# Optimization experiments

Measured on AMD Instinct MI355X. Metric: run time of the kernel, lower is better.

## Reference

```python
import jax, jax.numpy as jnp
import numpy as np

S, B, D, V = 1024, 8, 512, 8000


def _ln(x, g, b, eps=1e-5):
    m = x.mean(-1, keepdims=True)
    v = x.var(-1, keepdims=True)
    return (x - m) / jnp.sqrt(v + eps) * g + b


def setup_inputs() -> dict:
    key = jax.random.key(0)
    ks = jax.random.split(key, 8)
    representation = jax.random.normal(ks[0], (S, B, D), jnp.float32)
    # CTC-style logits: tokens come in runs of ~4 frames so argmax has segments
    tok = jax.random.randint(ks[1], (S // 4, B), 0, V)
    tok = jnp.repeat(tok, 4, axis=0)  # [S,B]
    logit = jax.random.normal(ks[2], (S, B, V), jnp.float32) + 6.0 * jax.nn.one_hot(tok, V, dtype=jnp.float32)
    padding = jnp.zeros((B, S), bool)  # all frames valid
    # linear_adapter: Linear(D,2D) -> ReLU -> Linear(2D,D) -> LayerNorm
    w1 = jax.random.normal(ks[3], (2 * D, D), jnp.float32) * (D ** -0.5)
    b1 = jnp.zeros((2 * D,), jnp.float32)
    w2 = jax.random.normal(ks[4], (D, 2 * D), jnp.float32) * ((2 * D) ** -0.5)
    b2 = jnp.zeros((D,), jnp.float32)
    ln1_g = jnp.ones((D,), jnp.float32)
    ln1_b = jnp.zeros((D,), jnp.float32)
    # embed_adapter weight [dict_size, dim], init std = dim**-0.5
    emb_w = jax.random.normal(ks[5], (V, D), jnp.float32) * (D ** -0.5)
    eln_g = jnp.ones((D,), jnp.float32)
    eln_b = jnp.zeros((D,), jnp.float32)
    return dict(representation=representation, logit=logit, padding=padding,
                w1=w1, b1=b1, w2=w2, b2=b2, ln1_g=ln1_g, ln1_b=ln1_b,
                emb_w=emb_w, eln_g=eln_g, eln_b=eln_b)


def reference(representation, logit, padding, w1, b1, w2, b2, ln1_g, ln1_b, emb_w, eln_g, eln_b):
    # distribution = softmax(logit / T), T = 1.0
    dist = jax.nn.softmax(logit, axis=-1)  # [S,B,V]
    # linear adapter: Linear -> ReLU -> Linear -> LN
    h = jax.nn.relu(jnp.einsum('sbd,ed->sbe', representation, w1) + b1)
    linear_out = _ln(jnp.einsum('sbe,de->sbd', h, w2) + b2, ln1_g, ln1_b)
    # context adapter: dist @ embed_adapter.weight, then embed LN
    soft_out = _ln(jnp.einsum('sbv,vd->sbd', dist, emb_w), eln_g, eln_b)
    out = linear_out + soft_out  # league
    # --- CTC 'avg' compress (shrink), vectorized; output padded to S frames ---
    pred = jnp.argmax(dist, axis=-1).T  # [B,S]
    valid = ~padding  # [B,S]
    prev = jnp.concatenate([jnp.full((pred.shape[0], 1), -1, pred.dtype), pred[:, :-1]], axis=1)
    change = (pred != prev) & valid  # segment starts
    seg = jnp.cumsum(change, axis=1) - 1  # segment id per frame
    seg = jnp.where(valid, seg, S)  # invalid frames -> out-of-range id
    # weights_matrix[b, t, s] = 1/len(segment s) if frame t in segment s
    onehot = (seg[:, :, None] == jnp.arange(S)[None, None, :]).astype(out.dtype)  # [B,S,S]
    counts = onehot.sum(1)  # [B,S] frames per segment
    w = onehot * jnp.where(counts > 0, 1.0 / counts, 0.0)[:, None, :]
    # representation.permute(1,2,0).bmm(weights).permute(2,0,1)
    compressed = jnp.einsum('sbd,bst->tbd', out, w)  # [S_new(padded to S), B, D]
    new_lengths = change.sum(1)
    new_padding = jnp.arange(S)[None, :] >= new_lengths[:, None]
    return compressed, new_padding
```

## Files before the change

kernel.cpp:

```cpp
#include <hip/hip_runtime.h>
#include <hip/hip_bf16.h>

typedef __attribute__((ext_vector_type(8))) __bf16 bf16x8;
typedef __attribute__((ext_vector_type(4))) __bf16 bf16x4;
typedef __attribute__((ext_vector_type(4))) float  f32x4;

#define AS1 __attribute__((address_space(1)))
#define AS3 __attribute__((address_space(3)))

__global__ __launch_bounds__(256) void k_prep(const float* __restrict__ rep,
                                              const float* __restrict__ w1,
                                              const float* __restrict__ w2,
                                              const float* __restrict__ emb,
                                              __bf16* __restrict__ Xb,
                                              __bf16* __restrict__ w1b,
                                              __bf16* __restrict__ w2b,
                                              __bf16* __restrict__ embT) {
  __shared__ float t[32][33];
  int bid = blockIdx.x;
  if (bid < 5120) {
    const float* in; __bf16* out; int i;
    if (bid < 4096)      { in = rep; out = Xb;  i = bid * 256 + threadIdx.x; }
    else if (bid < 4608) { in = w1;  out = w1b; i = (bid - 4096) * 256 + threadIdx.x; }
    else                 { in = w2;  out = w2b; i = (bid - 4608) * 256 + threadIdx.x; }
    float4 f = reinterpret_cast<const float4*>(in)[i];
    bf16x4 o = { (__bf16)f.x, (__bf16)f.y, (__bf16)f.z, (__bf16)f.w };
    reinterpret_cast<bf16x4*>(out)[i] = o;
  } else {
    int b2 = bid - 5120;
    int bi = b2 % 250, bj = b2 / 250;
    int c = threadIdx.x & 31, r8 = threadIdx.x >> 5;
#pragma unroll
    for (int i = 0; i < 4; ++i) {
      int r = r8 + i * 8;
      t[r][c] = emb[(size_t)(bi * 32 + r) * 512 + bj * 32 + c];
    }
    __syncthreads();
#pragma unroll
    for (int i = 0; i < 4; ++i) {
      int r = r8 + i * 8;
      embT[(size_t)(bj * 32 + r) * 8000 + bi * 32 + c] = (__bf16)t[c][r];
    }
  }
}

__global__ __launch_bounds__(256) void k_pack(const __bf16* __restrict__ embT,
                                              __bf16* __restrict__ embP) {
  int idx = blockIdx.x * 256 + threadIdx.x;
  int L = idx & 63;
  int gt = idx >> 6;
  int T = gt % 250, g = gt / 250;
  bf16x8 v = *(const bf16x8*)(embT + (size_t)(g * 16 + (L & 15)) * 8000 + T * 32 + (L >> 4) * 8);
  *(bf16x8*)(embP + (size_t)idx * 8) = v;
}

__global__ __launch_bounds__(512, 4) void k_fused(const float* __restrict__ logit,
                                                  const __bf16* __restrict__ embP,
                                                  __bf16* __restrict__ sofp,
                                                  float* __restrict__ rowsum,
                                                  float* __restrict__ amaxv,
                                                  int* __restrict__ amaxi) {
  __shared__ __align__(16) __bf16 lA[2][64 * 32];
  const int klen = 2016;
  int bid = blockIdx.x;
  int xcd = bid & 7;
  int chunk = xcd >> 1;
  int mb = ((bid >> 3) << 1) | (xcd & 1);
  int k0 = chunk * klen;
  int kn = min(klen, 8000 - k0);
  int nt = kn >> 5;
  int T0 = chunk * 63;
  int tid = threadIdx.x, lane = tid & 63, wid = tid >> 6;
  int ar = tid >> 3, ac = tid & 7;
  const float* lrow = logit + (size_t)(mb * 64 + ar) * 8000 + k0 + ac * 4;
  int awoff = ar * 64 + ((((ac >> 1) ^ ((ar >> 1) & 3)) << 4)) + (ac & 1) * 8;
  f32x4 acc[4][4] = {};
  float sumacc = 0.f, mv = -1e30f; int mi = 0;

  auto exppack = [&](float4 lg, int tt) -> bf16x4 {
    float e[4];
#pragma unroll
    for (int c = 0; c < 4; ++c) {
      float x = (&lg.x)[c];
      if (x > mv) { mv = x; mi = k0 + tt * 32 + ac * 4 + c; }
      e[c] = __expf(x);
      sumacc += e[c];
    }
    return bf16x4{ (__bf16)e[0], (__bf16)e[1], (__bf16)e[2], (__bf16)e[3] };
  };
  bf16x8 bcur[4];
  auto loadB = [&](int TT) {
#pragma unroll
    for (int n = 0; n < 4; ++n)
      bcur[n] = *(const bf16x8*)(embP + ((size_t)((wid * 4 + n) * 250 + TT)) * 512 + lane * 8);
  };

  float4 rb_ = *(const float4*)(lrow);
  float4 rb  = *(const float4*)(lrow + 32);
  loadB(T0);
  bf16x4 e0 = exppack(rb_, 0);
  *(bf16x4*)((char*)(&lA[0][0]) + awoff) = e0;

  int cur = 0;
  for (int t = 0; t < nt; ++t) {
    bool hn = (t + 1 < nt), h2 = (t + 2 < nt);
    float4 rc = rb;
    if (h2) rc = *(const float4*)(lrow + (size_t)(t + 2) * 32);
    asm volatile("s_waitcnt lgkmcnt(0)" ::: "memory");
    __builtin_amdgcn_s_barrier();
    if (hn) {
      bf16x4 e4 = exppack(rb, t + 1);
      *(bf16x4*)((char*)(&lA[cur ^ 1][0]) + awoff) = e4;
    }
    bf16x8 af[4];
#pragma unroll
    for (int m = 0; m < 4; ++m) {
      int r = m * 16 + (lane & 15);
      int s = (lane >> 4) ^ ((r >> 1) & 3);
      af[m] = *(const bf16x8*)((const char*)lA[cur] + r * 64 + s * 16);
    }
    __builtin_amdgcn_s_setprio(1);
#pragma unroll
    for (int m = 0; m < 4; ++m)
#pragma unroll
      for (int n = 0; n < 4; ++n)
        acc[m][n] = __builtin_amdgcn_mfma_f32_16x16x32_bf16(af[m], bcur[n], acc[m][n], 0, 0, 0);
    __builtin_amdgcn_s_setprio(0);
    if (hn) loadB(T0 + t + 1);
    rb = rc;
    cur ^= 1;
  }
#pragma unroll
  for (int o = 1; o <= 4; o <<= 1) {
    sumacc += __shfl_xor(sumacc, o);
    float ov = __shfl_xor(mv, o); int oi = __shfl_xor(mi, o);
    if (ov > mv || (ov == mv && oi < mi)) { mv = ov; mi = oi; }
  }
  int grow = mb * 64 + ar;
  if (ac == 0) {
    rowsum[chunk * 8192 + grow] = sumacc;
    amaxv[chunk * 8192 + grow]  = mv;
    amaxi[chunk * 8192 + grow]  = mi;
  }
  __bf16* Cb = sofp + (size_t)chunk * 8192 * 512;
  int row0 = mb * 64 + ((lane >> 4) << 2);
  int col0 = wid * 64 + (lane & 15);
#pragma unroll
  for (int n = 0; n < 4; ++n) {
    int col = col0 + n * 16;
#pragma unroll
    for (int m = 0; m < 4; ++m)
#pragma unroll
      for (int j = 0; j < 4; ++j)
        Cb[(size_t)(row0 + m * 16 + j) * 512 + col] = (__bf16)acc[m][n][j];
  }
}

template<int EPI>
__global__ __launch_bounds__(256) void k_gemm_bt(const __bf16* __restrict__ A,
                                                 const __bf16* __restrict__ B,
                                                 __bf16* __restrict__ Cb,
                                                 const float* __restrict__ bias,
                                                 int K, int N, int klen, long long ostride) {
  __shared__ __align__(16) __bf16 lA[2][128 * 64];
  __shared__ __align__(16) __bf16 lB[2][128 * 64];
  int tid = threadIdx.x, lane = tid & 63, wid = tid >> 6;
  int wr = wid >> 1, wc = wid & 1;
  int k0 = blockIdx.z * klen;
  int kn = min(klen, K - k0);
  int nt = kn >> 6;
  const __bf16* Ab = A + (size_t)blockIdx.x * 128 * K + k0;
  const __bf16* Bb = B + (size_t)blockIdx.y * 128 * K + k0;
  int sr = tid >> 3, ss = tid & 7;
  f32x4 acc[4][4] = {};

  auto stage = [&](int buf, int kt) {
#pragma unroll
    for (int i = 0; i < 4; ++i) {
      int r = i * 32 + sr;
      int col = kt + ((ss ^ (r & 7)) << 3);
      __builtin_amdgcn_global_load_lds((const AS1 void*)(Ab + (size_t)r * K + col),
                                       (AS3 void*)(&lA[buf][i * 2048 + tid * 8]), 16, 0, 0);
      __builtin_amdgcn_global_load_lds((const AS1 void*)(Bb + (size_t)r * K + col),
                                       (AS3 void*)(&lB[buf][i * 2048 + tid * 8]), 16, 0, 0);
    }
  };

  stage(0, 0);
  __syncthreads();
  int cur = 0;
  for (int t = 0; t < nt; ++t) {
    if (t + 1 < nt) stage(cur ^ 1, (t + 1) << 6);
#pragma unroll
    for (int kk = 0; kk < 2; ++kk) {
      bf16x8 af[4], bv[4];
#pragma unroll
      for (int m = 0; m < 4; ++m) {
        int r = wr * 64 + m * 16 + (lane & 15);
        int slot = ((kk << 2) + (lane >> 4)) ^ (r & 7);
        af[m] = *(const bf16x8*)((const char*)lA[cur] + r * 128 + slot * 16);
      }
#pragma unroll
      for (int n = 0; n < 4; ++n) {
        int r = wc * 64 + n * 16 + (lane & 15);
        int slot = ((kk << 2) + (lane >> 4)) ^ (r & 7);
        bv[n] = *(const bf16x8*)((const char*)lB[cur] + r * 128 + slot * 16);
      }
#pragma unroll
      for (int m = 0; m < 4; ++m)
#pragma unroll
        for (int n = 0; n < 4; ++n)
          acc[m][n] = __builtin_amdgcn_mfma_f32_16x16x32_bf16(af[m], bv[n], acc[m][n], 0, 0, 0);
    }
    __syncthreads();
    cur ^= 1;
  }
  if (EPI == 0) Cb += (size_t)blockIdx.z * (size_t)ostride;
  int row0 = blockIdx.x * 128 + wr * 64 + ((lane >> 4) << 2);
  int col0 = blockIdx.y * 128 + wc * 64 + (lane & 15);
#pragma unroll
  for (int n = 0; n < 4; ++n) {
    int col = col0 + n * 16;
    float bvv = (EPI == 1) ? bias[col] : 0.f;
#pragma unroll
    for (int m = 0; m < 4; ++m) {
#pragma unroll
      for (int j = 0; j < 4; ++j) {
        int row = row0 + m * 16 + j;
        float val = acc[m][n][j] + bvv;
        if (EPI == 1) val = fmaxf(val, 0.f);
        Cb[(size_t)row * N + col] = (__bf16)val;
      }
    }
  }
}

__global__ __launch_bounds__(256) void k_scan(const float* __restrict__ amaxv,
                                              const int* __restrict__ amaxi,
                                              int* __restrict__ seg_start,
                                              int* __restrict__ seg_cnt,
                                              int* __restrict__ new_len,
                                              float* __restrict__ out_pad) {
  __shared__ int lp[8192];
  __shared__ int len_s[8];
  int tid = threadIdx.x;
  for (int i = tid; i < 8192; i += 256) {
    float bv = amaxv[i]; int bi = amaxi[i];
#pragma unroll
    for (int c = 1; c < 4; ++c) {
      float v = amaxv[c * 8192 + i]; int ix = amaxi[c * 8192 + i];
      if (v > bv || (v == bv && ix < bi)) { bv = v; bi = ix; }
    }
    lp[(i & 7) * 1024 + (i >> 3)] = bi;
  }
  __syncthreads();
  if (tid < 8) {
    int b = tid, prev = -1, seg = -1, start = 0;
    const int* row = lp + b * 1024;
    for (int s = 0; s < 1024; ++s) {
      int p = row[s];
      if (p != prev) {
        if (seg >= 0) seg_cnt[b * 1024 + seg] = s - start;
        ++seg; seg_start[b * 1024 + seg] = s; start = s; prev = p;
      }
    }
    seg_cnt[b * 1024 + seg] = 1024 - start;
    len_s[b] = seg + 1;
    new_len[b] = seg + 1;
  }
  __syncthreads();
  for (int i = tid; i < 8192; i += 256) {
    int b = i >> 10, s = i & 1023;
    out_pad[b * 1024 + s] = (s >= len_s[b]) ? 1.f : 0.f;
  }
}

__global__ __launch_bounds__(256) void k_compress(const __bf16* __restrict__ lin,
                                                  const __bf16* __restrict__ sof,
                                                  const float* __restrict__ rowsum,
                                                  const float* __restrict__ bias2,
                                                  const float* __restrict__ g1, const float* __restrict__ b1,
                                                  const float* __restrict__ g2, const float* __restrict__ b2,
                                                  const int* __restrict__ seg_start,
                                                  const int* __restrict__ seg_cnt,
                                                  const int* __restrict__ new_len,
                                                  float* __restrict__ comp) {
  const long long P = (long long)8192 * 512;
  int wid = threadIdx.x >> 6, lane = threadIdx.x & 63;
  int t = blockIdx.x * 4 + wid, b = blockIdx.y;
  float* dst = comp + ((size_t)(t * 8 + b)) * 512 + lane * 8;
  int len = new_len[b];
  if (t >= len) {
    f32x4 z = {0.f, 0.f, 0.f, 0.f};
    *(f32x4*)dst = z; *(f32x4*)(dst + 4) = z;
    return;
  }
  int s0i = seg_start[b * 1024 + t], cnt = seg_cnt[b * 1024 + t];
  int d8 = lane * 8;
  float gg1[8], bbv1[8], gg2[8], bbv2[8], bb2v[8];
#pragma unroll
  for (int k = 0; k < 8; ++k) {
    gg1[k] = g1[d8 + k]; bbv1[k] = b1[d8 + k];
    gg2[k] = g2[d8 + k]; bbv2[k] = b2[d8 + k];
    bb2v[k] = bias2[d8 + k];
  }
  f32x4 a0 = {0.f, 0.f, 0.f, 0.f}, a1 = {0.f, 0.f, 0.f, 0.f};
  for (int s = s0i; s < s0i + cnt; ++s) {
    int row = s * 8 + b;
    size_t base = (size_t)row * 512 + d8;
    float invd = 1.f / (rowsum[row] + rowsum[8192 + row] + rowsum[16384 + row] + rowsum[24576 + row]);
    bf16x8 l0 = *(const bf16x8*)(lin + base);
    bf16x8 l1 = *(const bf16x8*)(lin + P + base);
    bf16x8 t0 = *(const bf16x8*)(sof + base);
    bf16x8 t1 = *(const bf16x8*)(sof + P + base);
    bf16x8 t2 = *(const bf16x8*)(sof + 2 * P + base);
    bf16x8 t3 = *(const bf16x8*)(sof + 3 * P + base);
    float x[8], y[8];
#pragma unroll
    for (int k = 0; k < 8; ++k) {
      x[k] = (float)l0[k] + (float)l1[k] + bb2v[k];
      y[k] = ((float)t0[k] + (float)t1[k] + (float)t2[k] + (float)t3[k]) * invd;
    }
    float sx = 0, qx = 0, sy = 0, qy = 0;
#pragma unroll
    for (int k = 0; k < 8; ++k) { sx += x[k]; qx += x[k] * x[k]; sy += y[k]; qy += y[k] * y[k]; }
#pragma unroll
    for (int o = 32; o; o >>= 1) {
      sx += __shfl_xor(sx, o); qx += __shfl_xor(qx, o);
      sy += __shfl_xor(sy, o); qy += __shfl_xor(qy, o);
    }
    const float invD = 1.f / 512.f;
    float mx = sx * invD, vx = qx * invD - mx * mx;
    float my = sy * invD, vy = qy * invD - my * my;
    float rx = rsqrtf(vx + 1e-5f), ry = rsqrtf(vy + 1e-5f);
#pragma unroll
    for (int k = 0; k < 8; ++k) {
      float o8 = (x[k] - mx) * rx * gg1[k] + bbv1[k] + (y[k] - my) * ry * gg2[k] + bbv2[k];
      if (k < 4) a0[k] += o8; else a1[k - 4] += o8;
    }
  }
  float inv = 1.f / (float)cnt;
  a0 *= inv; a1 *= inv;
  *(f32x4*)dst = a0; *(f32x4*)(dst + 4) = a1;
}

extern "C" void kernel_launch(void* const* d_in, const int* in_sizes, int n_in,
                              void* d_out, int out_size, void* d_ws, size_t ws_size,
                              hipStream_t stream) {
  const float* rep   = (const float*)d_in[0];
  const float* logit = (const float*)d_in[1];
  const float* w1    = (const float*)d_in[3];
  const float* b1    = (const float*)d_in[4];
  const float* w2    = (const float*)d_in[5];
  const float* b2    = (const float*)d_in[6];
  const float* g1    = (const float*)d_in[7];
  const float* bb1   = (const float*)d_in[8];
  const float* emb   = (const float*)d_in[9];
  const float* g2    = (const float*)d_in[10];
  const float* bb2   = (const float*)d_in[11];
  float* out = (float*)d_out;
  (void)in_sizes; (void)n_in; (void)out_size; (void)ws_size;

  char* ws = (char*)d_ws;
  size_t off = 0;
  auto alloc = [&](size_t bytes) -> void* {
    void* p = ws + off; off += (bytes + 255) & ~(size_t)255; return p;
  };
  const long long P = (long long)8192 * 512;
  __bf16* Xb    = (__bf16*)alloc((size_t)P * 2);
  __bf16* w1b   = (__bf16*)alloc((size_t)1024 * 512 * 2);
  __bf16* w2b   = (__bf16*)alloc((size_t)512 * 1024 * 2);
  __bf16* embT  = (__bf16*)alloc((size_t)512 * 8000 * 2);
  __bf16* embP  = (__bf16*)alloc((size_t)512 * 8000 * 2);
  __bf16* Hb    = (__bf16*)alloc((size_t)8192 * 1024 * 2);
  __bf16* linp  = (__bf16*)alloc((size_t)P * 2 * 2);
  __bf16* sofp  = (__bf16*)alloc((size_t)P * 2 * 4);
  float*  rowsm = (float*)alloc((size_t)4 * 8192 * 4);
  float*  amv   = (float*)alloc((size_t)4 * 8192 * 4);
  int*    ami   = (int*)alloc((size_t)4 * 8192 * 4);
  int*    segs  = (int*)alloc((size_t)8192 * 4);
  int*    segc  = (int*)alloc((size_t)8192 * 4);
  int*    nlen  = (int*)alloc(64);

  k_prep<<<9120, 256, 0, stream>>>(rep, w1, w2, emb, Xb, w1b, w2b, embT);
  k_pack<<<2000, 256, 0, stream>>>(embT, embP);
  k_fused<<<512, 512, 0, stream>>>(logit, embP, sofp, rowsm, amv, ami);
  k_gemm_bt<1><<<dim3(64, 8, 1), 256, 0, stream>>>(Xb, w1b, Hb, b1, 512, 1024, 512, 0);
  k_gemm_bt<0><<<dim3(64, 4, 2), 256, 0, stream>>>(Hb, w2b, linp, nullptr, 1024, 512, 512, P);
  k_scan<<<1, 256, 0, stream>>>(amv, ami, segs, segc, nlen, out + (size_t)8192 * 512);
  k_compress<<<dim3(256, 8), 256, 0, stream>>>(linp, sofp, rowsm, b2, g1, bb1, g2, bb2,
                                               segs, segc, nlen, out);
}
```

Baseline: 286.3 us.

## Pack embedding directly from fp32 and deepen logit/B prefetch in fused kernel

```diff
diff --git a/kernel.cpp b/kernel.cpp
--- a/kernel.cpp
+++ b/kernel.cpp
@@ -11,47 +11,33 @@
 __global__ __launch_bounds__(256) void k_prep(const float* __restrict__ rep,
                                               const float* __restrict__ w1,
                                               const float* __restrict__ w2,
-                                              const float* __restrict__ emb,
                                               __bf16* __restrict__ Xb,
                                               __bf16* __restrict__ w1b,
-                                              __bf16* __restrict__ w2b,
-                                              __bf16* __restrict__ embT) {
-  __shared__ float t[32][33];
+                                              __bf16* __restrict__ w2b) {
   int bid = blockIdx.x;
-  if (bid < 5120) {
-    const float* in; __bf16* out; int i;
-    if (bid < 4096)      { in = rep; out = Xb;  i = bid * 256 + threadIdx.x; }
-    else if (bid < 4608) { in = w1;  out = w1b; i = (bid - 4096) * 256 + threadIdx.x; }
-    else                 { in = w2;  out = w2b; i = (bid - 4608) * 256 + threadIdx.x; }
-    float4 f = reinterpret_cast<const float4*>(in)[i];
-    bf16x4 o = { (__bf16)f.x, (__bf16)f.y, (__bf16)f.z, (__bf16)f.w };
-    reinterpret_cast<bf16x4*>(out)[i] = o;
-  } else {
-    int b2 = bid - 5120;
-    int bi = b2 % 250, bj = b2 / 250;
-    int c = threadIdx.x & 31, r8 = threadIdx.x >> 5;
-#pragma unroll
-    for (int i = 0; i < 4; ++i) {
-      int r = r8 + i * 8;
-      t[r][c] = emb[(size_t)(bi * 32 + r) * 512 + bj * 32 + c];
-    }
-    __syncthreads();
-#pragma unroll
-    for (int i = 0; i < 4; ++i) {
-      int r = r8 + i * 8;
-      embT[(size_t)(bj * 32 + r) * 8000 + bi * 32 + c] = (__bf16)t[c][r];
-    }
-  }
-}
-
-__global__ __launch_bounds__(256) void k_pack(const __bf16* __restrict__ embT,
+  const float* in; __bf16* out; int i;
+  if (bid < 4096)      { in = rep; out = Xb;  i = bid * 256 + threadIdx.x; }
+  else if (bid < 4608) { in = w1;  out = w1b; i = (bid - 4096) * 256 + threadIdx.x; }
+  else                 { in = w2;  out = w2b; i = (bid - 4608) * 256 + threadIdx.x; }
+  float4 f = reinterpret_cast<const float4*>(in)[i];
+  bf16x4 o = { (__bf16)f.x, (__bf16)f.y, (__bf16)f.z, (__bf16)f.w };
+  reinterpret_cast<bf16x4*>(out)[i] = o;
+}
+
+__global__ __launch_bounds__(256) void k_pack(const float* __restrict__ emb,
                                               __bf16* __restrict__ embP) {
   int idx = blockIdx.x * 256 + threadIdx.x;
   int L = idx & 63;
   int gt = idx >> 6;
   int T = gt % 250, g = gt / 250;
-  bf16x8 v = *(const bf16x8*)(embT + (size_t)(g * 16 + (L & 15)) * 8000 + T * 32 + (L >> 4) * 8);
-  *(bf16x8*)(embP + (size_t)idx * 8) = v;
+  int kb = T * 32 + (L >> 4) * 8;
+  int d  = g * 16 + (L & 15);
+  float v[8];
+#pragma unroll
+  for (int j = 0; j < 8; ++j) v[j] = emb[(size_t)(kb + j) * 512 + d];
+  bf16x8 o = {(__bf16)v[0], (__bf16)v[1], (__bf16)v[2], (__bf16)v[3],
+              (__bf16)v[4], (__bf16)v[5], (__bf16)v[6], (__bf16)v[7]};
+  *(bf16x8*)(embP + (size_t)idx * 8) = o;
 }
 
 __global__ __launch_bounds__(512, 4) void k_fused(const float* __restrict__ logit,
@@ -88,30 +74,36 @@
     }
     return bf16x4{ (__bf16)e[0], (__bf16)e[1], (__bf16)e[2], (__bf16)e[3] };
   };
-  bf16x8 bcur[4];
-  auto loadB = [&](int TT) {
+  bf16x8 bcur[4], bnxt[4];
+  auto loadB = [&](bf16x8* dst, int TT) {
 #pragma unroll
     for (int n = 0; n < 4; ++n)
-      bcur[n] = *(const bf16x8*)(embP + ((size_t)((wid * 4 + n) * 250 + TT)) * 512 + lane * 8);
-  };
-
-  float4 rb_ = *(const float4*)(lrow);
-  float4 rb  = *(const float4*)(lrow + 32);
-  loadB(T0);
-  bf16x4 e0 = exppack(rb_, 0);
+      dst[n] = *(const bf16x8*)(embP + ((size_t)((wid * 4 + n) * 250 + TT)) * 512 + lane * 8);
+  };
+  auto loadR = [&](int i) -> float4 {
+    return *(const float4*)(lrow + (size_t)i * 32);
+  };
+
+  float4 r0 = loadR(0);
+  loadB(bcur, T0);
+  bf16x4 e0 = exppack(r0, 0);
   *(bf16x4*)((char*)(&lA[0][0]) + awoff) = e0;
+  float4 q0 = loadR(min(1, nt - 1));
+  float4 q1 = loadR(min(2, nt - 1));
+  float4 q2 = loadR(min(3, nt - 1));
+  float4 q3 = loadR(min(4, nt - 1));
 
   int cur = 0;
   for (int t = 0; t < nt; ++t) {
-    bool hn = (t + 1 < nt), h2 = (t + 2 < nt);
-    float4 rc = rb;
-    if (h2) rc = *(const float4*)(lrow + (size_t)(t + 2) * 32);
+    bool hn = (t + 1 < nt);
     asm volatile("s_waitcnt lgkmcnt(0)" ::: "memory");
     __builtin_amdgcn_s_barrier();
+    loadB(bnxt, min(T0 + t + 1, T0 + nt - 1));
     if (hn) {
-      bf16x4 e4 = exppack(rb, t + 1);
+      bf16x4 e4 = exppack(q0, t + 1);
       *(bf16x4*)((char*)(&lA[cur ^ 1][0]) + awoff) = e4;
     }
+    float4 qn = loadR(min(t + 5, nt - 1));
     bf16x8 af[4];
 #pragma unroll
     for (int m = 0; m < 4; ++m) {
@@ -126,8 +118,9 @@
       for (int n = 0; n < 4; ++n)
         acc[m][n] = __builtin_amdgcn_mfma_f32_16x16x32_bf16(af[m], bcur[n], acc[m][n], 0, 0, 0);
     __builtin_amdgcn_s_setprio(0);
-    if (hn) loadB(T0 + t + 1);
-    rb = rc;
+    q0 = q1; q1 = q2; q2 = q3; q3 = qn;
+#pragma unroll
+    for (int n = 0; n < 4; ++n) bcur[n] = bnxt[n];
     cur ^= 1;
   }
 #pragma unroll
@@ -370,7 +363,6 @@
   __bf16* Xb    = (__bf16*)alloc((size_t)P * 2);
   __bf16* w1b   = (__bf16*)alloc((size_t)1024 * 512 * 2);
   __bf16* w2b   = (__bf16*)alloc((size_t)512 * 1024 * 2);
-  __bf16* embT  = (__bf16*)alloc((size_t)512 * 8000 * 2);
   __bf16* embP  = (__bf16*)alloc((size_t)512 * 8000 * 2);
   __bf16* Hb    = (__bf16*)alloc((size_t)8192 * 1024 * 2);
   __bf16* linp  = (__bf16*)alloc((size_t)P * 2 * 2);
@@ -382,8 +374,8 @@
   int*    segc  = (int*)alloc((size_t)8192 * 4);
   int*    nlen  = (int*)alloc(64);
 
-  k_prep<<<9120, 256, 0, stream>>>(rep, w1, w2, emb, Xb, w1b, w2b, embT);
-  k_pack<<<2000, 256, 0, stream>>>(embT, embP);
+  k_prep<<<5120, 256, 0, stream>>>(rep, w1, w2, Xb, w1b, w2b);
+  k_pack<<<2000, 256, 0, stream>>>(emb, embP);
   k_fused<<<512, 512, 0, stream>>>(logit, embP, sofp, rowsm, amv, ami);
   k_gemm_bt<1><<<dim3(64, 8, 1), 256, 0, stream>>>(Xb, w1b, Hb, b1, 512, 1024, 512, 0);
   k_gemm_bt<0><<<dim3(64, 4, 2), 256, 0, stream>>>(Hb, w2b, linp, nullptr, 1024, 512, 512, P);
```

Measured after the change: 425.3 us. 1.49x slower.
